# Kernel optimization log

Hardware: AMD Instinct MI355X
Metric: run time of the kernel (lower is better)

The kernel has to match this reference:

```python
import jax, jax.numpy as jnp
import numpy as np

NUM_HEADS = 8
HEAD_DIM = 128
MAX_RES = 224.0


def rope_embed(feat_shape, dim, max_res=MAX_RES):
    # timm pixel_freq_bands: 2**linspace(0, log2(max_res)-1, dim//4) * pi
    num_bands = dim // 4
    bands = (2.0 ** jnp.linspace(0.0, float(np.log2(max_res)) - 1.0, num_bands)) * jnp.pi
    # pixel coords in [-1, 1] per spatial dim
    coords = [jnp.linspace(-1.0, 1.0, s) for s in feat_shape]
    grid = jnp.stack(jnp.meshgrid(*coords, indexing='ij'), axis=-1)[..., None]  # [H,W,2,1]
    pos = grid * bands  # [H,W,2,num_bands]
    n = int(np.prod(feat_shape))
    sin = jnp.repeat(jnp.sin(pos).reshape(n, -1), 2, axis=-1)  # [n, dim]
    cos = jnp.repeat(jnp.cos(pos).reshape(n, -1), 2, axis=-1)  # [n, dim]
    return sin, cos


def _rot(x):
    # interleaved rotate-half: (x0,x1,x2,x3,...) -> (-x1,x0,-x3,x2,...)
    return jnp.stack([-x[..., 1::2], x[..., ::2]], axis=-1).reshape(x.shape)


def setup_inputs() -> dict:
    key = jax.random.key(0)
    k1, k2, k3, k4 = jax.random.split(key, 4)
    C, E = 1024, 1024
    x = jax.random.normal(k1, (64, C, 16, 16), dtype=jnp.float32)
    qkv_w = jax.random.normal(k2, (3 * E, C), dtype=jnp.float32) * (C ** -0.5)
    qkv_b = jnp.zeros((3 * E,), dtype=jnp.float32)
    proj_w = jax.random.normal(k3, (E, E), dtype=jnp.float32) * (E ** -0.5)
    proj_b = jax.random.normal(k4, (E,), dtype=jnp.float32) * 0.02
    return {"x": x, "qkv_w": qkv_w, "qkv_b": qkv_b, "proj_w": proj_w, "proj_b": proj_b}


def reference(x, qkv_w, qkv_b, proj_w, proj_b):
    B, C, H, W = x.shape
    n = H * W
    scale = HEAD_DIM ** -0.5
    sin_emb, cos_emb = rope_embed((H, W), HEAD_DIM)  # [n, head_dim]

    t = x.reshape(B, C, n).transpose(0, 2, 1)                      # [B, n, C]
    t = jnp.concatenate([t.mean(axis=1, keepdims=True), t], axis=1)  # [B, n+1, C]

    qkv = t @ qkv_w.T + qkv_b                                      # [B, n+1, 3E]
    qkv = qkv.reshape(B, n + 1, 3, NUM_HEADS, HEAD_DIM).transpose(2, 0, 3, 1, 4)
    q, k, v = qkv[0], qkv[1], qkv[2]                               # [B, h, n+1, d]

    def apply_rope(z):
        zc, zs = z[:, :, :1], z[:, :, 1:]
        zs = zs * cos_emb + _rot(zs) * sin_emb
        return jnp.concatenate([zc, zs], axis=2)

    q = apply_rope(q)
    k = apply_rope(k)

    attn = jax.nn.softmax(jnp.einsum('bhqd,bhkd->bhqk', q, k) * scale, axis=-1)
    out = jnp.einsum('bhqk,bhkd->bhqd', attn, v)
    out = out.transpose(0, 2, 1, 3).reshape(B, n + 1, -1)           # [B, n+1, E]
    out = out @ proj_w.T + proj_b
    return out[:, 0]
```

## Files before the change

### kernel.cpp

```cpp
#include <hip/hip_runtime.h>
#include <math.h>

#define PI_F 3.14159265358979323846f
#define KSTEP 0.21959209425992272f

using bf16x8 = __attribute__((ext_vector_type(8))) short;
using f32x4 = __attribute__((ext_vector_type(4))) float;
using u16x8 = __attribute__((ext_vector_type(8))) unsigned short;

static __device__ __forceinline__ float wave_reduce_sum(float v) {
#pragma unroll
  for (int off = 32; off; off >>= 1) v += __shfl_down(v, off);
  return v;
}

static __device__ __forceinline__ unsigned short f2bf(float f) {
  unsigned u = __float_as_uint(f);
  return (unsigned short)((u + 0x7fffu + ((u >> 16) & 1u)) >> 16);
}

static __device__ __forceinline__ float bf2f(unsigned short s) {
  return __uint_as_float(((unsigned)s) << 16);
}

__global__ __launch_bounds__(256) void prep_kernel(const float* __restrict__ x,
                                                   const float* __restrict__ qkv_w,
                                                   const float* __restrict__ qkv_b,
                                                   unsigned short* __restrict__ xt,
                                                   float* __restrict__ t_mean,
                                                   unsigned short* __restrict__ wkT,
                                                   float2* __restrict__ sc) {
  const int bid = blockIdx.x;
  const int t = threadIdx.x;
  __shared__ float tile[64 * 33];
  __shared__ float tl2[64 * 65];
  if (bid < 1024) {
    const int ct = bid & 15, b = bid >> 4;
    const int cl = t >> 2, pq = (t & 3) * 8;
    const int pl = t >> 3, cq = (t & 7) * 8;
    float sum = 0.0f;
    const float* xrow = x + ((size_t)(b * 1024 + ct * 64 + cl) * 256) + pq;
    unsigned short* xtb = xt + (size_t)b * 262144 + ct * 64;
    for (int pt = 0; pt < 8; ++pt) {
      const float4 v0 = *reinterpret_cast<const float4*>(xrow + pt * 32);
      const float4 v1 = *reinterpret_cast<const float4*>(xrow + pt * 32 + 4);
      tile[cl * 33 + pq + 0] = v0.x; tile[cl * 33 + pq + 1] = v0.y;
      tile[cl * 33 + pq + 2] = v0.z; tile[cl * 33 + pq + 3] = v0.w;
      tile[cl * 33 + pq + 4] = v1.x; tile[cl * 33 + pq + 5] = v1.y;
      tile[cl * 33 + pq + 6] = v1.z; tile[cl * 33 + pq + 7] = v1.w;
      sum += (v0.x + v0.y) + (v0.z + v0.w) + (v1.x + v1.y) + (v1.z + v1.w);
      __syncthreads();
      u16x8 o;
#pragma unroll
      for (int e = 0; e < 8; ++e) o[e] = f2bf(tile[(cq + e) * 33 + pl]);
      *reinterpret_cast<u16x8*>(xtb + (size_t)(pt * 32 + pl) * 1024 + cq) = o;
      __syncthreads();
    }
    sum += __shfl_xor(sum, 1);
    sum += __shfl_xor(sum, 2);
    if ((t & 3) == 0) t_mean[b * 1024 + ct * 64 + cl] = sum * (1.0f / 256.0f);
  } else if (bid < 1280) {
    const int bb = bid - 1024;
    const int h = bb >> 5, t5 = bb & 31;
    const int dt = t5 >> 4, ct = t5 & 15;
    {
      const int dl = t >> 2, cq = (t & 3) * 16;
      const float* src = qkv_w + (size_t)(1024 + h * 128 + dt * 64 + dl) * 1024 + ct * 64 + cq;
#pragma unroll
      for (int i = 0; i < 4; ++i) {
        const float4 v = *reinterpret_cast<const float4*>(src + i * 4);
        tl2[dl * 65 + cq + i * 4 + 0] = v.x; tl2[dl * 65 + cq + i * 4 + 1] = v.y;
        tl2[dl * 65 + cq + i * 4 + 2] = v.z; tl2[dl * 65 + cq + i * 4 + 3] = v.w;
      }
    }
    __syncthreads();
    {
      const int cl = t >> 2, dq = (t & 3) * 16;
      unsigned short* dst = wkT + (size_t)(h * 1152 + ct * 64 + cl) * 128 + dt * 64 + dq;
      u16x8 o0, o1;
#pragma unroll
      for (int e = 0; e < 8; ++e) {
        o0[e] = f2bf(tl2[(dq + e) * 65 + cl]);
        o1[e] = f2bf(tl2[(dq + 8 + e) * 65 + cl]);
      }
      *reinterpret_cast<u16x8*>(dst) = o0;
      *reinterpret_cast<u16x8*>(dst + 8) = o1;
    }
  } else {
    const int idx = (bid - 1280) * 256 + t;
    const int m = idx >> 8, j = idx & 255;
    const float band = exp2f((float)(m & 31) * KSTEP) * PI_F;
    const float coord = (m < 32) ? (-1.0f + (2.0f / 15.0f) * (float)(j >> 4))
                                 : (-1.0f + (2.0f / 15.0f) * (float)(j & 15));
    float sn, cs;
    sincosf(coord * band, &sn, &cs);
    sc[idx] = make_float2(sn, cs);
  }
}

__global__ __launch_bounds__(256) void gemm_splitk(
    const float* __restrict__ A, int lda, int aStrideZ,
    const float* __restrict__ B, int ldb, int bStrideZ,
    float* __restrict__ Cp, int ldc, int cStrideZ, int cStrideKc, int KC) {
  const int nt = blockIdx.x, mt = blockIdx.y;
  const int z = blockIdx.z / KC, kc = blockIdx.z % KC;
  const int tid = threadIdx.x;
  A += (size_t)z * aStrideZ + (size_t)mt * 32 * lda + kc * 256;
  B += (size_t)z * bStrideZ + (size_t)nt * 64 * ldb + kc * 256;
  Cp += (size_t)kc * cStrideKc + (size_t)z * cStrideZ + (size_t)mt * 32 * ldc + nt * 64;

  __shared__ float As[32][34];
  __shared__ float Bs[32][68];

  const int tm = tid >> 4;
  const int tn = tid & 15;
  float acc0[4] = {0, 0, 0, 0}, acc1[4] = {0, 0, 0, 0};

  for (int k0 = 0; k0 < 256; k0 += 32) {
    {
      const int m = tid >> 3, kq = tid & 7;
      float4 v = *reinterpret_cast<const float4*>(A + (size_t)m * lda + k0 + kq * 4);
      As[kq * 4 + 0][m] = v.x; As[kq * 4 + 1][m] = v.y;
      As[kq * 4 + 2][m] = v.z; As[kq * 4 + 3][m] = v.w;
    }
#pragma unroll
    for (int r = 0; r < 2; ++r) {
      const int idx = r * 256 + tid;
      const int n = idx >> 3, kq = idx & 7;
      float4 v = *reinterpret_cast<const float4*>(B + (size_t)n * ldb + k0 + kq * 4);
      Bs[kq * 4 + 0][n] = v.x; Bs[kq * 4 + 1][n] = v.y;
      Bs[kq * 4 + 2][n] = v.z; Bs[kq * 4 + 3][n] = v.w;
    }
    __syncthreads();
#pragma unroll
    for (int k = 0; k < 32; ++k) {
      const float a0 = As[k][tm * 2], a1 = As[k][tm * 2 + 1];
      const float4 bb = *reinterpret_cast<const float4*>(&Bs[k][tn * 4]);
      acc0[0] += a0 * bb.x; acc0[1] += a0 * bb.y; acc0[2] += a0 * bb.z; acc0[3] += a0 * bb.w;
      acc1[0] += a1 * bb.x; acc1[1] += a1 * bb.y; acc1[2] += a1 * bb.z; acc1[3] += a1 * bb.w;
    }
    __syncthreads();
  }
  *reinterpret_cast<float4*>(Cp + (size_t)(tm * 2) * ldc + tn * 4) =
      make_float4(acc0[0], acc0[1], acc0[2], acc0[3]);
  *reinterpret_cast<float4*>(Cp + (size_t)(tm * 2 + 1) * ldc + tn * 4) =
      make_float4(acc1[0], acc1[1], acc1[2], acc1[3]);
}

__global__ __launch_bounds__(256) void gemm_proj_splitk(
    const float* __restrict__ Apart, const float* __restrict__ abias,
    const float* __restrict__ B, float* __restrict__ Cp) {
  const int nt = blockIdx.x, mt = blockIdx.y, kc = blockIdx.z;
  const int tid = threadIdx.x;
  B += (size_t)nt * 64 * 1024 + kc * 256;
  Cp += (size_t)kc * 65536 + (size_t)mt * 32 * 1024 + nt * 64;

  __shared__ float As[32][34];
  __shared__ float Bs[32][68];

  const int tm = tid >> 4;
  const int tn = tid & 15;
  float acc0[4] = {0, 0, 0, 0}, acc1[4] = {0, 0, 0, 0};

  for (int k0 = 0; k0 < 256; k0 += 32) {
    {
      const int m = tid >> 3, kq = tid & 7;
      const int kg = kc * 256 + k0 + kq * 4;
      const float* Ab = Apart + (size_t)(mt * 32 + m) * 1024 + kg;
      float4 v = *reinterpret_cast<const float4*>(abias + kg);
#pragma unroll
      for (int r = 0; r < 4; ++r) {
        const float4 p = *reinterpret_cast<const float4*>(Ab + (size_t)r * 65536);
        v.x += p.x; v.y += p.y; v.z += p.z; v.w += p.w;
      }
      As[kq * 4 + 0][m] = v.x; As[kq * 4 + 1][m] = v.y;
      As[kq * 4 + 2][m] = v.z; As[kq * 4 + 3][m] = v.w;
    }
#pragma unroll
    for (int r = 0; r < 2; ++r) {
      const int idx = r * 256 + tid;
      const int n = idx >> 3, kq = idx & 7;
      float4 v = *reinterpret_cast<const float4*>(B + (size_t)n * 1024 + k0 + kq * 4);
      Bs[kq * 4 + 0][n] = v.x; Bs[kq * 4 + 1][n] = v.y;
      Bs[kq * 4 + 2][n] = v.z; Bs[kq * 4 + 3][n] = v.w;
    }
    __syncthreads();
#pragma unroll
    for (int k = 0; k < 32; ++k) {
      const float a0 = As[k][tm * 2], a1 = As[k][tm * 2 + 1];
      const float4 bb = *reinterpret_cast<const float4*>(&Bs[k][tn * 4]);
      acc0[0] += a0 * bb.x; acc0[1] += a0 * bb.y; acc0[2] += a0 * bb.z; acc0[3] += a0 * bb.w;
      acc1[0] += a1 * bb.x; acc1[1] += a1 * bb.y; acc1[2] += a1 * bb.z; acc1[3] += a1 * bb.w;
    }
    __syncthreads();
  }
  *reinterpret_cast<float4*>(Cp + (size_t)(tm * 2) * 1024 + tn * 4) =
      make_float4(acc0[0], acc0[1], acc0[2], acc0[3]);
  *reinterpret_cast<float4*>(Cp + (size_t)(tm * 2 + 1) * 1024 + tn * 4) =
      make_float4(acc1[0], acc1[1], acc1[2], acc1[3]);
}

__global__ __launch_bounds__(256) void reduce4_bias(const float* __restrict__ part,
                                                    const float* __restrict__ bias,
                                                    float* __restrict__ out) {
  const int i = blockIdx.x * 256 + threadIdx.x;
  out[i] = part[i] + part[i + 65536] + part[i + 131072] + part[i + 196608] + bias[i & 1023];
}

__global__ __launch_bounds__(512) void scores_u(
    const unsigned short* __restrict__ wkT, const unsigned short* __restrict__ xt,
    const float* __restrict__ q0p, const float* __restrict__ qkv_b,
    const float2* __restrict__ sc, const float* __restrict__ t_mean,
    float* __restrict__ u) {
  const int l = blockIdx.x;
  const int b = ((l >> 5) << 3) | (l & 7);
  const int ht = (l >> 3) & 3;
  const int tid = threadIdx.x;
  const int w = tid >> 6, lane = tid & 63;
  const int rgrp = lane >> 4;

  const int hh_ = (w & 3) >> 1, sgen = (w & 3) & 1, ctl = w >> 2;

  __shared__ __align__(16) char smem[33792];
  float* persist = reinterpret_cast<float*>(smem);
  float* q0l = persist;
  float* k0l = persist + 256;
  float* biasg = persist + 512;
  float* ps = persist + 576;
  float* smax = persist + 580;
  float* ssum = persist + 588;
  float* attnl = persist + 596;
  char* Bt0 = smem + 4864;
  char* Bt1 = smem + 8960;

  const unsigned short* xtb = xt + (size_t)b * 262144;

  if (tid < 256) {
    const float* qp = q0p + (size_t)b * 2048 + ht * 256 + tid;
    q0l[tid] = qkv_b[ht * 256 + tid] + qp[0] + qp[131072] + qp[262144] + qp[393216];
    const float* kp = qp + 1024;
    k0l[tid] = qkv_b[1024 + ht * 256 + tid] + kp[0] + kp[131072] + kp[262144] + kp[393216];
  }
  __syncthreads();

  bf16x8 rq[2];
  {
    const int v = lane & 15;
    const int jrep = sgen ? v : v * 16;
#pragma unroll
    for (int kk = 0; kk < 2; ++kk) {
#pragma unroll
      for (int e = 0; e < 8; e += 2) {
        const int d = kk * 32 + rgrp * 8 + e;
        const int p = d >> 1;
        const float qe = q0l[hh_ * 128 + sgen * 64 + 2 * p];
        const float qo = q0l[hh_ * 128 + sgen * 64 + 2 * p + 1];
        const float2 tt = sc[(sgen * 32 + p) * 256 + jrep];
        rq[kk][e] = (short)f2bf(qe * tt.y + qo * tt.x);
        rq[kk][e + 1] = (short)f2bf(qo * tt.y - qe * tt.x);
      }
    }
  }

  const int c_ = ctl * 16 + (lane & 15);
  const unsigned short* wrow =
      wkT + ((size_t)(ht * 2 + hh_) * 1152 + c_) * 128 + sgen * 64 + rgrp * 8;
  const unsigned short* arow0 = xtb + (size_t)(w * 32 + (lane & 15)) * 1024 + rgrp * 8;
  const unsigned short* arow1 = arow0 + 16 * 1024;

#define WLOAD(dst0, dst1, tt)                                                   \
  {                                                                             \
    const unsigned short* p_ = wrow + (size_t)(tt)*4096;                        \
    dst0 = *reinterpret_cast<const bf16x8*>(p_);                                \
    dst1 = *reinterpret_cast<const bf16x8*>(p_ + 32);                           \
  }
#define ALOAD(dst0, dst1, tt)                                                   \
  {                                                                             \
    dst0 = *reinterpret_cast<const bf16x8*>(arow0 + (tt)*32);                   \
    dst1 = *reinterpret_cast<const bf16x8*>(arow1 + (tt)*32);                   \
  }
#define BGEN(W0, W1, dstBt)                                                     \
  {                                                                             \
    f32x4 accg = {};                                                            \
    accg = __builtin_amdgcn_mfma_f32_16x16x32_bf16(W0, rq[0], accg, 0, 0, 0);   \
    accg = __builtin_amdgcn_mfma_f32_16x16x32_bf16(W1, rq[1], accg, 0, 0, 0);   \
    const int n_ = (w & 3) * 16 + (lane & 15);                                  \
    const int cslot_ = ctl * 2 + (rgrp >> 1);                                   \
    const unsigned u0_ =                                                        \
        (unsigned)f2bf(accg[0]) | ((unsigned)f2bf(accg[1]) << 16);              \
    const unsigned u1_ =                                                        \
        (unsigned)f2bf(accg[2]) | ((unsigned)f2bf(accg[3]) << 16);              \
    *reinterpret_cast<uint2*>((dstBt) + n_ * 64 +                               \
                              ((cslot_ ^ ((n_ >> 1) & 3)) << 4) +               \
                              (rgrp & 1) * 8) = make_uint2(u0_, u1_);           \
  }

  f32x4 acc[2][4] = {};
  bf16x8 af0c, af1c, af0n, af1n, wf0n, wf1n, wf0n2, wf1n2;
  {
    bf16x8 wf00, wf10;
    WLOAD(wf00, wf10, 0);
    BGEN(wf00, wf10, Bt0);
  }
  ALOAD(af0c, af1c, 0);
  WLOAD(wf0n, wf1n, 1);
  asm volatile("s_waitcnt lgkmcnt(0)" ::: "memory");
  __builtin_amdgcn_s_barrier();

  for (int t = 0; t < 32; ++t) {
    if (t < 31) {
      char* dst = ((t + 1) & 1) ? Bt1 : Bt0;
      BGEN(wf0n, wf1n, dst);
    }
    {
      const int ta = (t + 1 > 31) ? 31 : (t + 1);
      const int tw = (t + 2 > 31) ? 31 : (t + 2);
      ALOAD(af0n, af1n, ta);
      WLOAD(wf0n2, wf1n2, tw);
    }
    {
      const char* Bb = (t & 1) ? Bt1 : Bt0;
      bf16x8 bfr[4];
#pragma unroll
      for (int ni = 0; ni < 4; ++ni) {
        const int n = ni * 16 + (lane & 15);
        const int slot = rgrp ^ ((n >> 1) & 3);
        bfr[ni] = *reinterpret_cast<const bf16x8*>(Bb + n * 64 + (slot << 4));
      }
      __builtin_amdgcn_s_setprio(1);
#pragma unroll
      for (int ni = 0; ni < 4; ++ni) {
        acc[0][ni] = __builtin_amdgcn_mfma_f32_16x16x32_bf16(af0c, bfr[ni], acc[0][ni], 0, 0, 0);
        acc[1][ni] = __builtin_amdgcn_mfma_f32_16x16x32_bf16(af1c, bfr[ni], acc[1][ni], 0, 0, 0);
      }
      __builtin_amdgcn_s_setprio(0);
    }
    af0c = af0n; af1c = af1n;
    wf0n = wf0n2; wf1n = wf1n2;
    asm volatile("s_waitcnt lgkmcnt(0)" ::: "memory");
    __builtin_amdgcn_s_barrier();
    asm volatile("" ::: "memory");
  }
#undef WLOAD
#undef ALOAD
#undef BGEN

  __syncthreads();

  float* Sp = reinterpret_cast<float*>(smem + 13056);
  float* up2 = reinterpret_cast<float*>(smem + 17408);

#pragma unroll
  for (int mi = 0; mi < 2; ++mi)
#pragma unroll
    for (int ni = 0; ni < 4; ++ni)
#pragma unroll
      for (int rr = 0; rr < 4; ++rr) {
        const int j = w * 32 + mi * 16 + (rgrp << 2) + rr;
        const int col = ni * 16 + (lane & 15);
        const int s = (col >> 4) & 1;
        const int sel = s ? (j & 15) : (j >> 4);
        if ((col & 15) == sel) Sp[(j * 2 + (col >> 5)) * 2 + s] = acc[mi][ni][rr];
      }
  if (tid < 64) {
    const int h_ = tid >> 5, s_ = (tid >> 4) & 1, v_ = tid & 15;
    const float* bk = qkv_b + 1024 + (ht * 2 + h_) * 128 + s_ * 64;
    const int jrep = s_ ? v_ : v_ * 16;
    float a = 0.0f;
#pragma unroll 4
    for (int p = 0; p < 32; ++p) {
      const float qe = q0l[h_ * 128 + s_ * 64 + 2 * p];
      const float qo = q0l[h_ * 128 + s_ * 64 + 2 * p + 1];
      const float2 tt = sc[(s_ * 32 + p) * 256 + jrep];
      a += (qe * tt.y + qo * tt.x) * bk[2 * p] + (qo * tt.y - qe * tt.x) * bk[2 * p + 1];
    }
    biasg[tid] = a;
  }
  if (tid < 256) {
    float pr = q0l[tid] * k0l[tid];
    pr = wave_reduce_sum(pr);
    if (lane == 0) ps[w] = pr;
  }
  __syncthreads();

  const float scale = 0.08838834764831845f;
  float e0 = 0.0f, e1 = 0.0f, eb0 = 0.0f, eb1 = 0.0f;
  if (tid < 256) {
    const float va0 = scale * (Sp[tid * 4 + 0] + Sp[tid * 4 + 1] + biasg[tid >> 4] +
                               biasg[16 + (tid & 15)]);
    const float va1 = scale * (Sp[tid * 4 + 2] + Sp[tid * 4 + 3] + biasg[32 + (tid >> 4)] +
                               biasg[48 + (tid & 15)]);
    float vb0 = -3.0e38f, vb1 = -3.0e38f;
    if (tid == 0) {
      vb0 = scale * (ps[0] + ps[1]);
      vb1 = scale * (ps[2] + ps[3]);
    }
    float m0 = fmaxf(va0, vb0), m1 = fmaxf(va1, vb1);
#pragma unroll
    for (int off = 32; off; off >>= 1) {
      m0 = fmaxf(m0, __shfl_xor(m0, off));
      m1 = fmaxf(m1, __shfl_xor(m1, off));
    }
    if (lane == 0) { smax[w] = m0; smax[4 + w] = m1; }
  }
  __syncthreads();
  if (tid < 256) {
    const float g0 = fmaxf(fmaxf(smax[0], smax[1]), fmaxf(smax[2], smax[3]));
    const float g1 = fmaxf(fmaxf(smax[4], smax[5]), fmaxf(smax[6], smax[7]));
    const float va0 = scale * (Sp[tid * 4 + 0] + Sp[tid * 4 + 1] + biasg[tid >> 4] +
                               biasg[16 + (tid & 15)]);
    const float va1 = scale * (Sp[tid * 4 + 2] + Sp[tid * 4 + 3] + biasg[32 + (tid >> 4)] +
                               biasg[48 + (tid & 15)]);
    e0 = expf(va0 - g0);
    e1 = expf(va1 - g1);
    if (tid == 0) {
      eb0 = expf(scale * (ps[0] + ps[1]) - g0);
      eb1 = expf(scale * (ps[2] + ps[3]) - g1);
    }
    float s0 = e0 + eb0, s1 = e1 + eb1;
#pragma unroll
    for (int off = 32; off; off >>= 1) {
      s0 += __shfl_xor(s0, off);
      s1 += __shfl_xor(s1, off);
    }
    if (lane == 0) { ssum[w] = s0; ssum[4 + w] = s1; }
  }
  __syncthreads();
  if (tid < 256) {
    const float inv0 = 1.0f / (ssum[0] + ssum[1] + ssum[2] + ssum[3]);
    const float inv1 = 1.0f / (ssum[4] + ssum[5] + ssum[6] + ssum[7]);
    attnl[1 + tid] = e0 * inv0;
    attnl[257 + 1 + tid] = e1 * inv1;
    if (tid == 0) { attnl[0] = eb0 * inv0; attnl[257] = eb1 * inv1; }
  }
  __syncthreads();

  {
    const int jh = w >> 2, cq = w & 3;
    const int c0 = cq * 256 + lane * 4;
    float ua0[4] = {}, ua1[4] = {};
    const unsigned short* xr = xtb + c0;
    for (int jj = 0; jj < 128; ++jj) {
      const int j = jh * 128 + jj;
      const float a0 = attnl[1 + j];
      const float a1 = attnl[258 + j];
      const ushort4 v = *reinterpret_cast<const ushort4*>(xr + (size_t)j * 1024);
      const float xs[4] = {bf2f(v.x), bf2f(v.y), bf2f(v.z), bf2f(v.w)};
#pragma unroll
      for (int e = 0; e < 4; ++e) {
        ua0[e] += a0 * xs[e];
        ua1[e] += a1 * xs[e];
      }
    }
#pragma unroll
    for (int e = 0; e < 4; ++e) {
      up2[jh * 2048 + 0 * 1024 + c0 + e] = ua0[e];
      up2[jh * 2048 + 1 * 1024 + c0 + e] = ua1[e];
    }
  }
  __syncthreads();
#pragma unroll
  for (int r = 0; r < 4; ++r) {
    const int o = tid * 4 + r;
    const int h2 = o >> 10, c = o & 1023;
    float s = up2[h2 * 1024 + c] + up2[2048 + h2 * 1024 + c];
    s += attnl[h2 * 257] * t_mean[b * 1024 + c];
    u[((size_t)b * 8 + ht * 2 + h2) * 1024 + c] = s;
  }
}

extern "C" void kernel_launch(void* const* d_in, const int* in_sizes, int n_in,
                              void* d_out, int out_size, void* d_ws, size_t ws_size,
                              hipStream_t stream) {
  const float* x = (const float*)d_in[0];
  const float* qkv_w = (const float*)d_in[1];
  const float* qkv_b = (const float*)d_in[2];
  const float* proj_w = (const float*)d_in[3];
  const float* proj_b = (const float*)d_in[4];
  float* out = (float*)d_out;

  float* ws = (float*)d_ws;
  float* t_mean = ws;
  float* q0k0_part = ws + 65536;
  float* u = ws + 589824;
  float* out0_part = ws + 1114112;
  float* out_part = ws + 1376256;
  float2* sc = (float2*)(ws + 1638400);
  unsigned short* wkT = (unsigned short*)(ws + 1671168);
  unsigned short* x_t = (unsigned short*)(ws + 11698176);

  prep_kernel<<<1344, 256, 0, stream>>>(x, qkv_w, qkv_b, x_t, t_mean, wkT, sc);

  gemm_splitk<<<dim3(32, 2, 4), 256, 0, stream>>>(t_mean, 1024, 0, qkv_w, 1024, 0,
                                                  q0k0_part, 2048, 0, 131072, 4);

  scores_u<<<256, 512, 0, stream>>>(wkT, x_t, q0k0_part, qkv_b, sc, t_mean, u);

  gemm_splitk<<<dim3(2, 2, 32), 256, 0, stream>>>(u, 8192, 1024,
                                                  qkv_w + (size_t)2048 * 1024, 1024, 131072,
                                                  out0_part, 1024, 128, 65536, 4);

  gemm_proj_splitk<<<dim3(16, 2, 4), 256, 0, stream>>>(out0_part, qkv_b + 2048, proj_w, out_part);

  reduce4_bias<<<256, 256, 0, stream>>>(out_part, proj_b, out);
}
```

Measured before the change: 102.1 us.

## Split scores_u into one block per head, doubling grid and cutting shared memory

The attention-scores kernel now gives each block one head instead of two, which doubles the grid from 256 to 512 blocks. Shared memory shrinks from about 33 KB to 12.8 KB and launch bounds ask for 4 blocks per CU. The K loop is restructured to half as many iterations, each loading twice the A and W data. The intent is more parallelism and occupancy on the CUs, at the cost of each block re-reading the same x_t rows for a single head, which doubles that global traffic.

```diff
diff --git a/kernel.cpp b/kernel.cpp
--- a/kernel.cpp
+++ b/kernel.cpp
@@ -207,39 +207,38 @@
   out[i] = part[i] + part[i + 65536] + part[i + 131072] + part[i + 196608] + bias[i & 1023];
 }
 
-__global__ __launch_bounds__(512) void scores_u(
+__global__ __launch_bounds__(512, 4) void scores_u(
     const unsigned short* __restrict__ wkT, const unsigned short* __restrict__ xt,
     const float* __restrict__ q0p, const float* __restrict__ qkv_b,
     const float2* __restrict__ sc, const float* __restrict__ t_mean,
     float* __restrict__ u) {
   const int l = blockIdx.x;
-  const int b = ((l >> 5) << 3) | (l & 7);
-  const int ht = (l >> 3) & 3;
+  const int b = ((l >> 6) << 3) | (l & 7);
+  const int h = (l >> 3) & 7;
   const int tid = threadIdx.x;
   const int w = tid >> 6, lane = tid & 63;
   const int rgrp = lane >> 4;
-
-  const int hh_ = (w & 3) >> 1, sgen = (w & 3) & 1, ctl = w >> 2;
-
-  __shared__ __align__(16) char smem[33792];
+  const int sgen = w & 1, ctl = w >> 1;
+
+  __shared__ __align__(16) char smem[12800];
   float* persist = reinterpret_cast<float*>(smem);
   float* q0l = persist;
-  float* k0l = persist + 256;
-  float* biasg = persist + 512;
-  float* ps = persist + 576;
-  float* smax = persist + 580;
-  float* ssum = persist + 588;
-  float* attnl = persist + 596;
-  char* Bt0 = smem + 4864;
-  char* Bt1 = smem + 8960;
+  float* k0l = persist + 128;
+  float* biasg = persist + 256;
+  float* ps = persist + 288;
+  float* smax = persist + 290;
+  float* ssum = persist + 294;
+  float* attnl = persist + 298;
+  char* Bt0 = smem + 2560;
+  char* Bt1 = smem + 6656;
 
   const unsigned short* xtb = xt + (size_t)b * 262144;
 
-  if (tid < 256) {
-    const float* qp = q0p + (size_t)b * 2048 + ht * 256 + tid;
-    q0l[tid] = qkv_b[ht * 256 + tid] + qp[0] + qp[131072] + qp[262144] + qp[393216];
+  if (tid < 128) {
+    const float* qp = q0p + (size_t)b * 2048 + h * 128 + tid;
+    q0l[tid] = qkv_b[h * 128 + tid] + qp[0] + qp[131072] + qp[262144] + qp[393216];
     const float* kp = qp + 1024;
-    k0l[tid] = qkv_b[1024 + ht * 256 + tid] + kp[0] + kp[131072] + kp[262144] + kp[393216];
+    k0l[tid] = qkv_b[1024 + h * 128 + tid] + kp[0] + kp[131072] + kp[262144] + kp[393216];
   }
   __syncthreads();
 
@@ -253,8 +252,8 @@
       for (int e = 0; e < 8; e += 2) {
         const int d = kk * 32 + rgrp * 8 + e;
         const int p = d >> 1;
-        const float qe = q0l[hh_ * 128 + sgen * 64 + 2 * p];
-        const float qo = q0l[hh_ * 128 + sgen * 64 + 2 * p + 1];
+        const float qe = q0l[sgen * 64 + 2 * p];
+        const float qo = q0l[sgen * 64 + 2 * p + 1];
         const float2 tt = sc[(sgen * 32 + p) * 256 + jrep];
         rq[kk][e] = (short)f2bf(qe * tt.y + qo * tt.x);
         rq[kk][e + 1] = (short)f2bf(qo * tt.y - qe * tt.x);
@@ -262,80 +261,86 @@
     }
   }
 
-  const int c_ = ctl * 16 + (lane & 15);
   const unsigned short* wrow =
-      wkT + ((size_t)(ht * 2 + hh_) * 1152 + c_) * 128 + sgen * 64 + rgrp * 8;
-  const unsigned short* arow0 = xtb + (size_t)(w * 32 + (lane & 15)) * 1024 + rgrp * 8;
-  const unsigned short* arow1 = arow0 + 16 * 1024;
-
-#define WLOAD(dst0, dst1, tt)                                                   \
+      wkT + ((size_t)h * 1152 + ctl * 16 + (lane & 15)) * 128 + sgen * 64 + rgrp * 8;
+  const unsigned short* ar0 = xtb + (size_t)(w * 32 + (lane & 15)) * 1024 + rgrp * 8;
+  const unsigned short* ar1 = ar0 + 16 * 1024;
+
+#define WLOAD(d0, d1, tt)                                                       \
   {                                                                             \
-    const unsigned short* p_ = wrow + (size_t)(tt)*4096;                        \
-    dst0 = *reinterpret_cast<const bf16x8*>(p_);                                \
-    dst1 = *reinterpret_cast<const bf16x8*>(p_ + 32);                           \
-  }
-#define ALOAD(dst0, dst1, tt)                                                   \
+    const unsigned short* p_ = wrow + (size_t)(tt)*8192;                        \
+    d0 = *reinterpret_cast<const bf16x8*>(p_);                                  \
+    d1 = *reinterpret_cast<const bf16x8*>(p_ + 32);                             \
+  }
+#define ALOAD(a00, a01, a10, a11, tt)                                           \
   {                                                                             \
-    dst0 = *reinterpret_cast<const bf16x8*>(arow0 + (tt)*32);                   \
-    dst1 = *reinterpret_cast<const bf16x8*>(arow1 + (tt)*32);                   \
+    a00 = *reinterpret_cast<const bf16x8*>(ar0 + (tt)*64);                      \
+    a01 = *reinterpret_cast<const bf16x8*>(ar0 + (tt)*64 + 32);                 \
+    a10 = *reinterpret_cast<const bf16x8*>(ar1 + (tt)*64);                      \
+    a11 = *reinterpret_cast<const bf16x8*>(ar1 + (tt)*64 + 32);                 \
   }
 #define BGEN(W0, W1, dstBt)                                                     \
   {                                                                             \
     f32x4 accg = {};                                                            \
     accg = __builtin_amdgcn_mfma_f32_16x16x32_bf16(W0, rq[0], accg, 0, 0, 0);   \
     accg = __builtin_amdgcn_mfma_f32_16x16x32_bf16(W1, rq[1], accg, 0, 0, 0);   \
-    const int n_ = (w & 3) * 16 + (lane & 15);                                  \
+    const int n_ = sgen * 16 + (lane & 15);                                     \
     const int cslot_ = ctl * 2 + (rgrp >> 1);                                   \
     const unsigned u0_ =                                                        \
         (unsigned)f2bf(accg[0]) | ((unsigned)f2bf(accg[1]) << 16);              \
     const unsigned u1_ =                                                        \
         (unsigned)f2bf(accg[2]) | ((unsigned)f2bf(accg[3]) << 16);              \
-    *reinterpret_cast<uint2*>((dstBt) + n_ * 64 +                               \
-                              ((cslot_ ^ ((n_ >> 1) & 3)) << 4) +               \
+    *reinterpret_cast<uint2*>((dstBt) + n_ * 128 +                              \
+                              ((cslot_ ^ ((n_ >> 1) & 7)) << 4) +               \
                               (rgrp & 1) * 8) = make_uint2(u0_, u1_);           \
   }
 
-  f32x4 acc[2][4] = {};
-  bf16x8 af0c, af1c, af0n, af1n, wf0n, wf1n, wf0n2, wf1n2;
+  f32x4 acc[2][2] = {};
+  bf16x8 a00c, a01c, a10c, a11c, a00n, a01n, a10n, a11n;
+  bf16x8 wf0n, wf1n, wf0n2, wf1n2;
   {
-    bf16x8 wf00, wf10;
-    WLOAD(wf00, wf10, 0);
-    BGEN(wf00, wf10, Bt0);
-  }
-  ALOAD(af0c, af1c, 0);
+    bf16x8 w00, w10;
+    WLOAD(w00, w10, 0);
+    BGEN(w00, w10, Bt0);
+  }
+  ALOAD(a00c, a01c, a10c, a11c, 0);
   WLOAD(wf0n, wf1n, 1);
   asm volatile("s_waitcnt lgkmcnt(0)" ::: "memory");
   __builtin_amdgcn_s_barrier();
 
-  for (int t = 0; t < 32; ++t) {
-    if (t < 31) {
+  for (int t = 0; t < 16; ++t) {
+    if (t < 15) {
       char* dst = ((t + 1) & 1) ? Bt1 : Bt0;
       BGEN(wf0n, wf1n, dst);
     }
     {
-      const int ta = (t + 1 > 31) ? 31 : (t + 1);
-      const int tw = (t + 2 > 31) ? 31 : (t + 2);
-      ALOAD(af0n, af1n, ta);
+      const int ta = (t + 1 > 15) ? 15 : (t + 1);
+      const int tw = (t + 2 > 15) ? 15 : (t + 2);
+      ALOAD(a00n, a01n, a10n, a11n, ta);
       WLOAD(wf0n2, wf1n2, tw);
     }
     {
       const char* Bb = (t & 1) ? Bt1 : Bt0;
-      bf16x8 bfr[4];
-#pragma unroll
-      for (int ni = 0; ni < 4; ++ni) {
-        const int n = ni * 16 + (lane & 15);
-        const int slot = rgrp ^ ((n >> 1) & 3);
-        bfr[ni] = *reinterpret_cast<const bf16x8*>(Bb + n * 64 + (slot << 4));
-      }
+      bf16x8 bfr[2][2];
+#pragma unroll
+      for (int ni = 0; ni < 2; ++ni)
+#pragma unroll
+        for (int kk = 0; kk < 2; ++kk) {
+          const int n = ni * 16 + (lane & 15);
+          const int slot = (kk * 4 + rgrp) ^ ((n >> 1) & 7);
+          bfr[ni][kk] = *reinterpret_cast<const bf16x8*>(Bb + n * 128 + (slot << 4));
+        }
       __builtin_amdgcn_s_setprio(1);
 #pragma unroll
-      for (int ni = 0; ni < 4; ++ni) {
-        acc[0][ni] = __builtin_amdgcn_mfma_f32_16x16x32_bf16(af0c, bfr[ni], acc[0][ni], 0, 0, 0);
-        acc[1][ni] = __builtin_amdgcn_mfma_f32_16x16x32_bf16(af1c, bfr[ni], acc[1][ni], 0, 0, 0);
+      for (int ni = 0; ni < 2; ++ni) {
+        acc[0][ni] = __builtin_amdgcn_mfma_f32_16x16x32_bf16(a00c, bfr[ni][0], acc[0][ni], 0, 0, 0);
+        acc[0][ni] = __builtin_amdgcn_mfma_f32_16x16x32_bf16(a01c, bfr[ni][1], acc[0][ni], 0, 0, 0);
+        acc[1][ni] = __builtin_amdgcn_mfma_f32_16x16x32_bf16(a10c, bfr[ni][0], acc[1][ni], 0, 0, 0);
+        acc[1][ni] = __builtin_amdgcn_mfma_f32_16x16x32_bf16(a11c, bfr[ni][1], acc[1][ni], 0, 0, 0);
       }
       __builtin_amdgcn_s_setprio(0);
     }
-    af0c = af0n; af1c = af1n;
+    a00c = a00n; a01c = a01n; a10c = a10n; a11c = a11n;
     wf0n = wf0n2; wf1n = wf1n2;
     asm volatile("s_waitcnt lgkmcnt(0)" ::: "memory");
     __builtin_amdgcn_s_barrier();
@@ -347,36 +352,35 @@
 
   __syncthreads();
 
-  float* Sp = reinterpret_cast<float*>(smem + 13056);
-  float* up2 = reinterpret_cast<float*>(smem + 17408);
+  float* Sp = reinterpret_cast<float*>(smem + 10752);
+  float* up2 = reinterpret_cast<float*>(smem + 2560);
 
 #pragma unroll
   for (int mi = 0; mi < 2; ++mi)
 #pragma unroll
-    for (int ni = 0; ni < 4; ++ni)
+    for (int ni = 0; ni < 2; ++ni)
 #pragma unroll
       for (int rr = 0; rr < 4; ++rr) {
         const int j = w * 32 + mi * 16 + (rgrp << 2) + rr;
-        const int col = ni * 16 + (lane & 15);
-        const int s = (col >> 4) & 1;
-        const int sel = s ? (j & 15) : (j >> 4);
-        if ((col & 15) == sel) Sp[(j * 2 + (col >> 5)) * 2 + s] = acc[mi][ni][rr];
-      }
-  if (tid < 64) {
-    const int h_ = tid >> 5, s_ = (tid >> 4) & 1, v_ = tid & 15;
-    const float* bk = qkv_b + 1024 + (ht * 2 + h_) * 128 + s_ * 64;
+        const int v = lane & 15;
+        const int sel = ni ? (j & 15) : (j >> 4);
+        if (v == sel) Sp[j * 2 + ni] = acc[mi][ni][rr];
+      }
+  if (tid < 32) {
+    const int s_ = tid >> 4, v_ = tid & 15;
+    const float* bk = qkv_b + 1024 + h * 128 + s_ * 64;
     const int jrep = s_ ? v_ : v_ * 16;
     float a = 0.0f;
 #pragma unroll 4
     for (int p = 0; p < 32; ++p) {
-      const float qe = q0l[h_ * 128 + s_ * 64 + 2 * p];
-      const float qo = q0l[h_ * 128 + s_ * 64 + 2 * p + 1];
+      const float qe = q0l[s_ * 64 + 2 * p];
+      const float qo = q0l[s_ * 64 + 2 * p + 1];
       const float2 tt = sc[(s_ * 32 + p) * 256 + jrep];
       a += (qe * tt.y + qo * tt.x) * bk[2 * p] + (qo * tt.y - qe * tt.x) * bk[2 * p + 1];
     }
     biasg[tid] = a;
   }
-  if (tid < 256) {
+  if (tid < 128) {
     float pr = q0l[tid] * k0l[tid];
     pr = wave_reduce_sum(pr);
     if (lane == 0) ps[w] = pr;
@@ -384,88 +388,63 @@
   __syncthreads();
 
   const float scale = 0.08838834764831845f;
-  float e0 = 0.0f, e1 = 0.0f, eb0 = 0.0f, eb1 = 0.0f;
+  float ea = 0.0f, eb = 0.0f;
   if (tid < 256) {
-    const float va0 = scale * (Sp[tid * 4 + 0] + Sp[tid * 4 + 1] + biasg[tid >> 4] +
-                               biasg[16 + (tid & 15)]);
-    const float va1 = scale * (Sp[tid * 4 + 2] + Sp[tid * 4 + 3] + biasg[32 + (tid >> 4)] +
-                               biasg[48 + (tid & 15)]);
-    float vb0 = -3.0e38f, vb1 = -3.0e38f;
-    if (tid == 0) {
-      vb0 = scale * (ps[0] + ps[1]);
-      vb1 = scale * (ps[2] + ps[3]);
-    }
-    float m0 = fmaxf(va0, vb0), m1 = fmaxf(va1, vb1);
-#pragma unroll
-    for (int off = 32; off; off >>= 1) {
-      m0 = fmaxf(m0, __shfl_xor(m0, off));
-      m1 = fmaxf(m1, __shfl_xor(m1, off));
-    }
-    if (lane == 0) { smax[w] = m0; smax[4 + w] = m1; }
+    const float va = scale * (Sp[tid * 2] + Sp[tid * 2 + 1] + biasg[tid >> 4] +
+                              biasg[16 + (tid & 15)]);
+    float vb = -3.0e38f;
+    if (tid == 0) vb = scale * (ps[0] + ps[1]);
+    float m0 = fmaxf(va, vb);
+#pragma unroll
+    for (int off = 32; off; off >>= 1) m0 = fmaxf(m0, __shfl_xor(m0, off));
+    if (lane == 0) smax[w] = m0;
   }
   __syncthreads();
   if (tid < 256) {
     const float g0 = fmaxf(fmaxf(smax[0], smax[1]), fmaxf(smax[2], smax[3]));
-    const float g1 = fmaxf(fmaxf(smax[4], smax[5]), fmaxf(smax[6], smax[7]));
-    const float va0 = scale * (Sp[tid * 4 + 0] + Sp[tid * 4 + 1] + biasg[tid >> 4] +
-                               biasg[16 + (tid & 15)]);
-    const float va1 = scale * (Sp[tid * 4 + 2] + Sp[tid * 4 + 3] + biasg[32 + (tid >> 4)] +
-                               biasg[48 + (tid & 15)]);
-    e0 = expf(va0 - g0);
-    e1 = expf(va1 - g1);
-    if (tid == 0) {
-      eb0 = expf(scale * (ps[0] + ps[1]) - g0);
-      eb1 = expf(scale * (ps[2] + ps[3]) - g1);
-    }
-    float s0 = e0 + eb0, s1 = e1 + eb1;
-#pragma unroll
-    for (int off = 32; off; off >>= 1) {
-      s0 += __shfl_xor(s0, off);
-      s1 += __shfl_xor(s1, off);
-    }
-    if (lane == 0) { ssum[w] = s0; ssum[4 + w] = s1; }
+    const float va = scale * (Sp[tid * 2] + Sp[tid * 2 + 1] + biasg[tid >> 4] +
+                              biasg[16 + (tid & 15)]);
+    ea = expf(va - g0);
+    if (tid == 0) eb = expf(scale * (ps[0] + ps[1]) - g0);
+    float s0 = ea + eb;
+#pragma unroll
+    for (int off = 32; off; off >>= 1) s0 += __shfl_xor(s0, off);
+    if (lane == 0) ssum[w] = s0;
   }
   __syncthreads();
   if (tid < 256) {
-    const float inv0 = 1.0f / (ssum[0] + ssum[1] + ssum[2] + ssum[3]);
-    const float inv1 = 1.0f / (ssum[4] + ssum[5] + ssum[6] + ssum[7]);
-    attnl[1 + tid] = e0 * inv0;
-    attnl[257 + 1 + tid] = e1 * inv1;
-    if (tid == 0) { attnl[0] = eb0 * inv0; attnl[257] = eb1 * inv1; }
+    const float inv = 1.0f / (ssum[0] + ssum[1] + ssum[2] + ssum[3]);
+    attnl[1 + tid] = ea * inv;
+    if (tid == 0) attnl[0] = eb * inv;
   }
   __syncthreads();
 
   {
     const int jh = w >> 2, cq = w & 3;
     const int c0 = cq * 256 + lane * 4;
-    float ua0[4] = {}, ua1[4] = {};
+    float ua[4] = {};
     const unsigned short* xr = xtb + c0;
     for (int jj = 0; jj < 128; ++jj) {
       const int j = jh * 128 + jj;
       const float a0 = attnl[1 + j];
-      const float a1 = attnl[258 + j];
       const ushort4 v = *reinterpret_cast<const ushort4*>(xr + (size_t)j * 1024);
-      const float xs[4] = {bf2f(v.x), bf2f(v.y), bf2f(v.z), bf2f(v.w)};
-#pragma unroll
-      for (int e = 0; e < 4; ++e) {
-        ua0[e] += a0 * xs[e];
-        ua1[e] += a1 * xs[e];
-      }
-    }
-#pragma unroll
-    for (int e = 0; e < 4; ++e) {
-      up2[jh * 2048 + 0 * 1024 + c0 + e] = ua0[e];
-      up2[jh * 2048 + 1 * 1024 + c0 + e] = ua1[e];
-    }
-  }
-  __syncthreads();
-#pragma unroll
-  for (int r = 0; r < 4; ++r) {
-    const int o = tid * 4 + r;
-    const int h2 = o >> 10, c = o & 1023;
-    float s = up2[h2 * 1024 + c] + up2[2048 + h2 * 1024 + c];
-    s += attnl[h2 * 257] * t_mean[b * 1024 + c];
-    u[((size_t)b * 8 + ht * 2 + h2) * 1024 + c] = s;
+      ua[0] += a0 * bf2f(v.x);
+      ua[1] += a0 * bf2f(v.y);
+      ua[2] += a0 * bf2f(v.z);
+      ua[3] += a0 * bf2f(v.w);
+    }
+#pragma unroll
+    for (int e = 0; e < 4; ++e) up2[jh * 1024 + c0 + e] = ua[e];
+  }
+  __syncthreads();
+  if (tid < 256) {
+#pragma unroll
+    for (int r = 0; r < 4; ++r) {
+      const int c = tid * 4 + r;
+      float s = up2[c] + up2[1024 + c];
+      s += attnl[0] * t_mean[b * 1024 + c];
+      u[((size_t)b * 8 + h) * 1024 + c] = s;
+    }
   }
 }
 
@@ -494,7 +473,7 @@
   gemm_splitk<<<dim3(32, 2, 4), 256, 0, stream>>>(t_mean, 1024, 0, qkv_w, 1024, 0,
                                                   q0k0_part, 2048, 0, 131072, 4);
 
-  scores_u<<<256, 512, 0, stream>>>(wkT, x_t, q0k0_part, qkv_b, sc, t_mean, u);
+  scores_u<<<512, 512, 0, stream>>>(wkT, x_t, q0k0_part, qkv_b, sc, t_mean, u);
 
   gemm_splitk<<<dim3(2, 2, 32), 256, 0, stream>>>(u, 8192, 1024,
                                                   qkv_w + (size_t)2048 * 1024, 1024, 131072,
```

After: 121.0 us. 18.6% more time.
